# Kernel optimization log

Hardware: AMD Instinct MI355X
Metric: run time of the kernel (lower is better)

Reference implementation:

```python
import jax, jax.numpy as jnp
import numpy as np

SHAPE = (64, 64, 64)
N0 = 4000
K = 5  # subm conv kernel size -> 125 taps


def _neighbors(coors, shp):
    # coors: [N,4] int (b,z,y,x), batch=1. Returns [N,125] int32 neighbor row ids, -1 if absent.
    offs = np.stack(np.meshgrid(np.arange(-2, 3), np.arange(-2, 3), np.arange(-2, 3), indexing='ij'), -1).reshape(-1, 3)
    shp = np.asarray(shp)
    grid = -np.ones(tuple(shp), np.int32)
    grid[coors[:, 1], coors[:, 2], coors[:, 3]] = np.arange(len(coors), dtype=np.int32)
    nb = coors[:, None, 1:4] + offs[None]  # [N,125,3]
    valid = ((nb >= 0) & (nb < shp)).all(-1)
    nbc = np.clip(nb, 0, shp - 1)
    nbr = grid[nbc[..., 0], nbc[..., 1], nbc[..., 2]]
    return np.where(valid, nbr, -1).astype(np.int32)


def _pool_map(coors, shp):
    # kernel 2 stride 2 sparse max pool: parent cell = spatial // 2
    out_shp = [s // 2 for s in shp]
    sp = coors[:, 1:4] // 2
    lin = (sp[:, 0] * out_shp[1] + sp[:, 1]) * out_shp[2] + sp[:, 2]
    uniq, inv = np.unique(lin, return_inverse=True)
    z = uniq // (out_shp[1] * out_shp[2])
    r = uniq % (out_shp[1] * out_shp[2])
    nc = np.stack([np.zeros_like(z), z, r // out_shp[2], r % out_shp[2]], 1).astype(np.int32)
    return inv.astype(np.int32), nc, out_shp


_PAIRS = [(3, 64), (64, 64), (64, 96), (96, 96), (96, 128), (128, 128), (128, 160), (160, 160), (160, 192), (192, 192), (192, 224), (224, 224), (224, 256), (256, 256)]
_WNAMES = ['w0a', 'w0b', 'w1a', 'w1b', 'w2a', 'w2b', 'w3a', 'w3b', 'w4a', 'w4b', 'w5a', 'w5b', 'w6a', 'w6b']


def setup_inputs() -> dict:
    rng = np.random.RandomState(0)
    lin = rng.choice(SHAPE[0] * SHAPE[1] * SHAPE[2], N0, replace=False)
    z = lin // (SHAPE[1] * SHAPE[2])
    r = lin % (SHAPE[1] * SHAPE[2])
    coors = np.stack([np.zeros_like(z), z, r // SHAPE[2], r % SHAPE[2]], 1).astype(np.int32)
    inp = {}
    c, shp = coors, list(SHAPE)
    for l in range(7):
        inp['nbr%d' % l] = jnp.asarray(_neighbors(c, shp))
        if l < 6:
            pm, c, shp = _pool_map(c, shp)
            inp['pool%d' % l] = jnp.asarray(pm)
    key = jax.random.key(0)
    for name, (ci, co) in zip(_WNAMES, _PAIRS):
        key, k = jax.random.split(key)
        inp[name] = jax.random.normal(k, (K ** 3, ci, co), jnp.float32) * (K ** 3 * ci) ** -0.5
    key, kf = jax.random.split(key)
    inp['features'] = jax.random.normal(kf, (N0, 3), jnp.float32)
    inp['coors'] = jnp.asarray(coors)
    inp['batch_size'] = 1
    return inp


def _subm(feats, nbr, w):
    # gather-GEMM-scatter form of SubMConv3d (bias=False): out active set == in active set
    valid = nbr >= 0  # [N,125]
    g = jnp.take(feats, jnp.maximum(nbr, 0), axis=0)  # [N,125,Cin]
    g = jnp.where(valid[:, :, None], g, jnp.zeros((), feats.dtype))
    return jnp.einsum('nkc,kco->no', g, w)  # [N,Cout]


def reference(features, coors, batch_size, nbr0, nbr1, nbr2, nbr3, nbr4, nbr5, nbr6, pool0, pool1, pool2, pool3, pool4, pool5, w0a, w0b, w1a, w1b, w2a, w2b, w3a, w3b, w4a, w4b, w5a, w5b, w6a, w6b):
    nbrs = (nbr0, nbr1, nbr2, nbr3, nbr4, nbr5, nbr6)
    pools = (pool0, pool1, pool2, pool3, pool4, pool5)
    ws = ((w0a, w0b), (w1a, w1b), (w2a, w2b), (w3a, w3b), (w4a, w4b), (w5a, w5b), (w6a, w6b))
    x = features
    for l in range(7):
        x = _subm(x, nbrs[l], ws[l][0])
        x = _subm(x, nbrs[l], ws[l][1])
        if l < 6:
            # sparse max pool over active voxels of each 2x2x2 cell
            x = jax.ops.segment_max(x, pools[l], num_segments=nbrs[l + 1].shape[0])
    return x
```

## Files before the change

kernel.cpp:

```cpp
#include <hip/hip_runtime.h>
#include <stddef.h>
#include <stdint.h>

#define KTAPS 125

typedef _Float16 f16x8 __attribute__((ext_vector_type(8)));
typedef float    f32x4 __attribute__((ext_vector_type(4)));

template<int NT, bool F32IN>
__global__ __launch_bounds__(256) void subm_mfma(
    const void* __restrict__ fin, const int* __restrict__ nbr,
    const _Float16* __restrict__ wt, float* __restrict__ fout,
    int N, int CinP, int TS, int CS, float inscale, float outscale)
{
    constexpr int BN = NT * 32;
    __shared__ int       nbs[16][64];
    __shared__ unsigned  msk[16][2];
    __shared__ unsigned char vtl[2][16];
    __shared__ int       vcs[2];

    const int tid  = threadIdx.x;
    const int lane = tid & 63;
    const int wid  = tid >> 6;
    const int wy   = wid & 1;
    const int wx   = wid >> 1;
    const int r15  = lane & 15;
    const int g4   = lane >> 4;
    const int row0 = blockIdx.x * 64;
    const int k0   = (blockIdx.y * KTAPS) / TS;
    const int k1   = ((blockIdx.y + 1) * KTAPS) / TS;
    const int KR   = k1 - k0;
    const int CC   = CinP >> 5;
    const int cc0  = (blockIdx.z * CC) / CS;
    const int cc1  = ((blockIdx.z + 1) * CC) / CS;

    #pragma unroll
    for (int p = 0; p < 4; ++p) {
        int e = tid + p * 256;
        if (e < KR * 64) {
            int j = e >> 6, r = e & 63;
            int gr = row0 + r;
            nbs[j][r] = (gr < N) ? nbr[(size_t)gr * KTAPS + k0 + j] : -1;
        }
    }
    __syncthreads();
    for (int j = wid; j < KR; j += 4) {
        unsigned long long m = __ballot(nbs[j][lane] >= 0);
        if (lane == 0) { msk[j][0] = (unsigned)m; msk[j][1] = (unsigned)(m >> 32); }
    }
    __syncthreads();
    if (wid < 2) {
        int c = 0;
        for (int j = 0; j < KR; ++j)
            if (msk[j][wid]) { if (lane == 0) vtl[wid][c] = (unsigned char)j; ++c; }
        if (lane == 0) vcs[wid] = c;
    }
    __syncthreads();
    const int VCw = vcs[wy];
    if (VCw == 0) return;

    unsigned um = 0;
    for (int t = 0; t < VCw; ++t) um |= msk[vtl[wy][t]][wy];

    f32x4 acc[2][NT];
    #pragma unroll
    for (int mt = 0; mt < 2; ++mt)
        #pragma unroll
        for (int nf = 0; nf < NT; ++nf)
            acc[mt][nf] = (f32x4){0.f, 0.f, 0.f, 0.f};

    const size_t wchunk = (size_t)32 * BN;
    const int    boffh  = (g4 * BN + wx * (NT * 16) + r15) * 8;

    auto LOADA = [&](f16x8 (&a)[2], int j, int c) {
        #pragma unroll
        for (int mt = 0; mt < 2; ++mt) {
            int src = nbs[j][wy * 32 + mt * 16 + r15];
            if (src < 0) src = N;
            size_t base = (size_t)src * CinP + c * 32 + g4 * 8;
            if (F32IN) {
                const float* p = (const float*)fin + base;
                float4 v0 = *(const float4*)p;
                float4 v1 = *(const float4*)(p + 4);
                f16x8 h;
                h[0] = (_Float16)(v0.x * inscale); h[1] = (_Float16)(v0.y * inscale);
                h[2] = (_Float16)(v0.z * inscale); h[3] = (_Float16)(v0.w * inscale);
                h[4] = (_Float16)(v1.x * inscale); h[5] = (_Float16)(v1.y * inscale);
                h[6] = (_Float16)(v1.z * inscale); h[7] = (_Float16)(v1.w * inscale);
                a[mt] = h;
            } else {
                a[mt] = *(const f16x8*)((const _Float16*)fin + base);
            }
        }
    };
    auto LOADB = [&](f16x8 (&b)[NT], int j, int c) {
        const _Float16* base = wt + ((size_t)(k0 + j) * CC + c) * wchunk;
        #pragma unroll
        for (int nf = 0; nf < NT; ++nf)
            b[nf] = *(const f16x8*)&base[boffh + nf * 128];
    };
    auto MFMA = [&](f16x8 (&a)[2], f16x8 (&b)[NT]) {
        #pragma unroll
        for (int mt = 0; mt < 2; ++mt)
            #pragma unroll
            for (int nf = 0; nf < NT; ++nf)
                acc[mt][nf] = __builtin_amdgcn_mfma_f32_16x16x32_f16(a[mt], b[nf], acc[mt][nf], 0, 0, 0);
    };

    f16x8 a0[2], b0[NT], a1[2], b1[NT];
    int i = 0, c = cc0;
    { int j = vtl[wy][0]; LOADA(a0, j, c); LOADB(b0, j, c); }
    while (true) {
        int ni = i, nc = c + 1; if (nc == cc1) { ni = i + 1; nc = cc0; }
        bool m1 = ni < VCw;
        if (m1) { int j = vtl[wy][ni]; LOADA(a1, j, nc); LOADB(b1, j, nc); }
        MFMA(a0, b0);
        if (!m1) break;
        i = ni; c = nc;
        ni = i; nc = c + 1; if (nc == cc1) { ni = i + 1; nc = cc0; }
        bool m2 = ni < VCw;
        if (m2) { int j = vtl[wy][ni]; LOADA(a0, j, nc); LOADB(b0, j, nc); }
        MFMA(a1, b1);
        if (!m2) break;
        i = ni; c = nc;
    }

    #pragma unroll
    for (int mt = 0; mt < 2; ++mt) {
        #pragma unroll
        for (int q = 0; q < 4; ++q) {
            int lr = mt * 16 + g4 * 4 + q;
            int gr = row0 + wy * 32 + lr;
            if (((um >> lr) & 1u) && gr < N) {
                #pragma unroll
                for (int nf = 0; nf < NT; ++nf) {
                    int col = wx * (NT * 16) + nf * 16 + r15;
                    atomicAdd(&fout[(size_t)gr * BN + col], acc[mt][nf][q] * outscale);
                }
            }
        }
    }
}

__global__ __launch_bounds__(256) void tap_flags(
    const int* n0, const int* n1, const int* n2, const int* n3,
    const int* n4, const int* n5, const int* n6,
    int N0, int N1, int N2, int N3, int N4, int N5, int N6,
    unsigned* __restrict__ flags)
{
    int l = blockIdx.y, k = blockIdx.x;
    const int* nb; int N;
    switch (l) {
        case 0: nb = n0; N = N0; break;  case 1: nb = n1; N = N1; break;
        case 2: nb = n2; N = N2; break;  case 3: nb = n3; N = N3; break;
        case 4: nb = n4; N = N4; break;  case 5: nb = n5; N = N5; break;
        default: nb = n6; N = N6; break;
    }
    bool any = false;
    for (int r = threadIdx.x; r < N; r += 256) any |= (nb[(size_t)r * KTAPS + k] >= 0);
    bool a = __syncthreads_or(any);
    if (threadIdx.x == 0) flags[l * KTAPS + k] = a ? 1u : 0u;
}

__global__ __launch_bounds__(256) void cvt_weights(
    const float* __restrict__ wa, const float* __restrict__ wb,
    _Float16* __restrict__ ta, _Float16* __restrict__ tb,
    const unsigned* __restrict__ flags,
    int CinA, int CCa, int CoutA, int splitA,
    int CinB, int CCb, int CoutB)
{
    int k = blockIdx.x;
    if (!flags[k]) return;
    int by = blockIdx.y;
    const float* w; _Float16* t; int Cin, CC, Cout, cc, c0;
    if (by < splitA) { w = wa; t = ta; Cin = CinA; CC = CCa; Cout = CoutA;
                       cc = by / (CoutA / 32); c0 = (by % (CoutA / 32)) * 32; }
    else { by -= splitA; w = wb; t = tb; Cin = CinB; CC = CCb; Cout = CoutB;
           cc = by / (CoutB / 32); c0 = (by % (CoutB / 32)) * 32; }

    __shared__ float T[32][33];
    int tid = threadIdx.x;
    #pragma unroll
    for (int p = 0; p < 4; ++p) {
        int e = tid + p * 256;
        int r = e >> 5, cl = e & 31;
        int ci = cc * 32 + r;
        T[r][cl] = (ci < Cin) ? w[((size_t)k * Cin + ci) * Cout + c0 + cl] : 0.f;
    }
    __syncthreads();
    if (tid < 128) {
        int g = tid >> 5, co = tid & 31;
        f16x8 h;
        #pragma unroll
        for (int j = 0; j < 8; ++j) h[j] = (_Float16)T[g * 8 + j][co];
        *(f16x8*)&t[((size_t)k * CC + cc) * (32 * (size_t)Cout) + ((size_t)g * Cout + c0 + co) * 8] = h;
    }
}

__global__ __launch_bounds__(256) void init_all(
    const float* __restrict__ feat, _Float16* __restrict__ H,
    float* __restrict__ Fa, float* __restrict__ Fb,
    unsigned* __restrict__ ENC, float* __restrict__ dout,
    int N0, int nFa, int nFb, int nE, int nOut)
{
    int i = blockIdx.x * 256 + threadIdx.x;
    if (i < nFa) Fa[i] = 0.f;
    if (i < nFb) Fb[i] = 0.f;
    if (i < nE)  ENC[i] = 0u;
    if (i < nOut) dout[i] = 0.f;
    int nH = (N0 + 1) * 32;
    if (i < nH) {
        int r = i >> 5, cl = i & 31;
        H[i] = (r < N0 && cl < 3) ? (_Float16)feat[r * 3 + cl] : (_Float16)0.f;
    }
}

__device__ __forceinline__ unsigned enc_f32(float f) {
    unsigned u = __float_as_uint(f);
    return (u & 0x80000000u) ? ~u : (u | 0x80000000u);
}

__global__ __launch_bounds__(256) void pool_max(
    float* __restrict__ Fb, const int* __restrict__ pm,
    unsigned* __restrict__ ENC, float* __restrict__ Fa,
    int Nin, int C, int nzero)
{
    int i = blockIdx.x * 256 + threadIdx.x;
    if (i < Nin * C) {
        int r = i / C, cl = i - r * C;
        atomicMax(&ENC[(size_t)pm[r] * C + cl], enc_f32(Fb[i]));
        Fb[i] = 0.f;
    }
    if (i < nzero) Fa[i] = 0.f;
}

__global__ __launch_bounds__(256) void pool_dec(
    unsigned* __restrict__ ENC, _Float16* __restrict__ H, int Nout, int C, float scale)
{
    int i = blockIdx.x * 256 + threadIdx.x;
    if (i < Nout * C) {
        unsigned u = ENC[i];
        float f = __uint_as_float((u & 0x80000000u) ? (u ^ 0x80000000u) : ~u);
        H[i] = (_Float16)(f * scale);
        ENC[i] = 0u;
    } else if (i < (Nout + 1) * C) {
        H[i] = (_Float16)0.f;
    }
}

template<bool F32>
static void conv_dispatch(int NT, dim3 g, hipStream_t s, const void* fin, const int* nbr,
                          const _Float16* wt, float* fout, int N, int CinP, int TS, int CS,
                          float insc, float outsc)
{
    switch (NT) {
        case 2: subm_mfma<2,F32><<<g,256,0,s>>>(fin,nbr,wt,fout,N,CinP,TS,CS,insc,outsc); break;
        case 3: subm_mfma<3,F32><<<g,256,0,s>>>(fin,nbr,wt,fout,N,CinP,TS,CS,insc,outsc); break;
        case 4: subm_mfma<4,F32><<<g,256,0,s>>>(fin,nbr,wt,fout,N,CinP,TS,CS,insc,outsc); break;
        case 5: subm_mfma<5,F32><<<g,256,0,s>>>(fin,nbr,wt,fout,N,CinP,TS,CS,insc,outsc); break;
        case 6: subm_mfma<6,F32><<<g,256,0,s>>>(fin,nbr,wt,fout,N,CinP,TS,CS,insc,outsc); break;
        case 7: subm_mfma<7,F32><<<g,256,0,s>>>(fin,nbr,wt,fout,N,CinP,TS,CS,insc,outsc); break;
        case 8: subm_mfma<8,F32><<<g,256,0,s>>>(fin,nbr,wt,fout,N,CinP,TS,CS,insc,outsc); break;
    }
}

static void launch_conv(bool f32in, const void* fin, const int* nbr, const _Float16* wt,
                        float* fout, int N, int CinP, int Cout, float insc, float outsc,
                        hipStream_t s)
{
    int rt = (N + 63) / 64;
    int TS = (1536 + rt - 1) / rt;
    if (TS > KTAPS) TS = KTAPS;
    int CC = CinP / 32;
    int CS = 1;
    long blocks = (long)rt * TS;
    if (blocks < 1024) { CS = (int)((1536 + blocks - 1) / blocks); if (CS > CC) CS = CC; }
    dim3 g(rt, TS, CS);
    if (f32in) conv_dispatch<true >(Cout/32, g, s, fin, nbr, wt, fout, N, CinP, TS, CS, insc, outsc);
    else       conv_dispatch<false>(Cout/32, g, s, fin, nbr, wt, fout, N, CinP, TS, CS, insc, outsc);
}

extern "C" void kernel_launch(void* const* d_in, const int* in_sizes, int n_in,
                              void* d_out, int out_size, void* d_ws, size_t ws_size,
                              hipStream_t stream)
{
    const int* nbr[7]; const int* pm[6]; int Ns[7];
    {
        int idx = 0;
        for (int l = 0; l < 7; ++l) {
            nbr[l] = (const int*)d_in[idx];
            Ns[l]  = in_sizes[idx] / KTAPS;
            ++idx;
            if (l < 6) { pm[l] = (const int*)d_in[idx]; ++idx; }
        }
    }
    const float* w[14];
    for (int i = 0; i < 14; ++i) w[i] = (const float*)d_in[13 + i];
    const float* feat = (const float*)d_in[27];

    static const int CI[14]  = {3,64, 64,96, 96,128, 128,160, 160,192, 192,224, 224,256};
    static const int CO[14]  = {64,64, 96,96, 128,128, 160,160, 192,192, 224,224, 256,256};
    static const int KSH[14] = {0,3, 2,2, 1,1, 0,0, 0,1, 0,2, 2,3};
    const float finalScale = 1.0f / 131072.0f;
    int CinP[14];
    for (int i = 0; i < 14; ++i) CinP[i] = (CI[i] < 32) ? 32 : CI[i];

    size_t maxFa = 0, maxFb = 0, maxE = 0, maxHa = 0, maxWA = 0, maxWB = 0;
    for (int l = 0; l < 7; ++l) {
        size_t fa = (size_t)(Ns[l] + 1) * CO[2*l];   if (fa > maxFa) maxFa = fa;
        size_t fb = (size_t)(Ns[l] + 1) * CO[2*l+1]; if (fb > maxFb) maxFb = fb;
        if (l < 6) { size_t e = (size_t)Ns[l+1] * CO[2*l+1]; if (e > maxE) maxE = e; }
        size_t ha = (size_t)(Ns[l] + 1) * CinP[2*l]; if (ha > maxHa) maxHa = ha;
        size_t wa = (size_t)KTAPS * CinP[2*l] * CO[2*l];     if (wa > maxWA) maxWA = wa;
        size_t wb = (size_t)KTAPS * CinP[2*l+1] * CO[2*l+1]; if (wb > maxWB) maxWB = wb;
    }
    size_t off = 0;
    auto carve = [&](size_t bytes) -> void* {
        void* p = (char*)d_ws + off;
        off = (off + bytes + 255) & ~(size_t)255;
        return p;
    };
    float*     Fa   = (float*)carve(maxFa * 4);
    float*     Fb   = (float*)carve(maxFb * 4);
    unsigned*  ENC  = (unsigned*)carve(maxE * 4);
    _Float16*  Ha   = (_Float16*)carve(maxHa * 2);
    _Float16*  wtA  = (_Float16*)carve(maxWA * 2);
    _Float16*  wtB  = (_Float16*)carve(maxWB * 2);
    unsigned*  flags= (unsigned*)carve(7 * KTAPS * 4);

    {
        int nMax = (int)maxFa;
        if ((int)maxFb > nMax) nMax = (int)maxFb;
        if ((int)maxE  > nMax) nMax = (int)maxE;
        int nH = (Ns[0] + 1) * 32;
        if (nH > nMax) nMax = nH;
        if (out_size > nMax) nMax = out_size;
        init_all<<<(nMax + 255) / 256, 256, 0, stream>>>(
            feat, Ha, Fa, Fb, ENC, (float*)d_out,
            Ns[0], (int)maxFa, (int)maxFb, (int)maxE, out_size);
    }
    tap_flags<<<dim3(KTAPS, 7), 256, 0, stream>>>(
        nbr[0], nbr[1], nbr[2], nbr[3], nbr[4], nbr[5], nbr[6],
        Ns[0], Ns[1], Ns[2], Ns[3], Ns[4], Ns[5], Ns[6], flags);

    for (int l = 0; l < 7; ++l) {
        int ia = 2 * l, ib = 2 * l + 1;
        int N = Ns[l];
        int splitA = (CinP[ia] / 32) * (CO[ia] / 32);
        int splitB = (CinP[ib] / 32) * (CO[ib] / 32);
        cvt_weights<<<dim3(KTAPS, splitA + splitB), 256, 0, stream>>>(
            w[ia], w[ib], wtA, wtB, flags + l * KTAPS,
            CI[ia], CinP[ia] / 32, CO[ia], splitA,
            CI[ib], CinP[ib] / 32, CO[ib]);

        launch_conv(false, Ha, nbr[l], wtA, Fa, N, CinP[ia], CO[ia], 1.f, 1.f, stream);

        float* outb = (l == 6) ? (float*)d_out : Fb;
        launch_conv(true, Fa, nbr[l], wtB, outb, N, CinP[ib], CO[ib],
                    (float)(1 << KSH[ib]), (l == 6) ? finalScale : 1.f, stream);

        if (l < 6) {
            int C = CO[ib], Nout = Ns[l + 1];
            int nzero = (Nout + 1) * CO[2 * l + 2];
            int tot = N * C; if (nzero > tot) tot = nzero;
            pool_max<<<(tot + 255) / 256, 256, 0, stream>>>(Fb, pm[l], ENC, Fa, N, C, nzero);
            int tot2 = (Nout + 1) * C;
            pool_dec<<<(tot2 + 255) / 256, 256, 0, stream>>>(ENC, Ha, Nout, C,
                                                             (float)(1 << KSH[2 * l + 2]));
        }
    }
}
```

Before: 427.2 us.

## Replace atomic split-K accumulation with per-split partial buffers and reduction kernels

The sparse conv kernel no longer uses atomicAdd into fp32 output. Each tap-split block now writes plain stores into its own partial-sum slice. New reduce kernels sum the slices, and they also fuse the fp16 conversion for the next conv and the encoded max-pool atomics, which removes the separate pool_max pass and the zeroing of accumulators. The channel-split grid dimension is dropped, and MFMAs and A-loads for all-empty 16-row halves are skipped. The cost is writing and re-reading TS×N×C fp32 partials, plus a different split-count heuristic.

```diff
diff --git a/kernel.cpp b/kernel.cpp
--- a/kernel.cpp
+++ b/kernel.cpp
@@ -3,15 +3,17 @@
 #include <stdint.h>
 
 #define KTAPS 125
+#define TARGET_BLOCKS 512
 
 typedef _Float16 f16x8 __attribute__((ext_vector_type(8)));
+typedef _Float16 f16x4 __attribute__((ext_vector_type(4)));
 typedef float    f32x4 __attribute__((ext_vector_type(4)));
 
-template<int NT, bool F32IN>
+template<int NT>
 __global__ __launch_bounds__(256) void subm_mfma(
-    const void* __restrict__ fin, const int* __restrict__ nbr,
-    const _Float16* __restrict__ wt, float* __restrict__ fout,
-    int N, int CinP, int TS, int CS, float inscale, float outscale)
+    const _Float16* __restrict__ finh, const int* __restrict__ nbr,
+    const _Float16* __restrict__ wt, float* __restrict__ Pout,
+    int N, int CinP, int TS)
 {
     constexpr int BN = NT * 32;
     __shared__ int       nbs[16][64];
@@ -31,8 +33,6 @@
     const int k1   = ((blockIdx.y + 1) * KTAPS) / TS;
     const int KR   = k1 - k0;
     const int CC   = CinP >> 5;
-    const int cc0  = (blockIdx.z * CC) / CS;
-    const int cc1  = ((blockIdx.z + 1) * CC) / CS;
 
     #pragma unroll
     for (int p = 0; p < 4; ++p) {
@@ -57,10 +57,6 @@
     }
     __syncthreads();
     const int VCw = vcs[wy];
-    if (VCw == 0) return;
-
-    unsigned um = 0;
-    for (int t = 0; t < VCw; ++t) um |= msk[vtl[wy][t]][wy];
 
     f32x4 acc[2][NT];
     #pragma unroll
@@ -69,76 +65,138 @@
         for (int nf = 0; nf < NT; ++nf)
             acc[mt][nf] = (f32x4){0.f, 0.f, 0.f, 0.f};
 
-    const size_t wchunk = (size_t)32 * BN;
-    const int    boffh  = (g4 * BN + wx * (NT * 16) + r15) * 8;
-
-    auto LOADA = [&](f16x8 (&a)[2], int j, int c) {
-        #pragma unroll
-        for (int mt = 0; mt < 2; ++mt) {
-            int src = nbs[j][wy * 32 + mt * 16 + r15];
-            if (src < 0) src = N;
-            size_t base = (size_t)src * CinP + c * 32 + g4 * 8;
-            if (F32IN) {
-                const float* p = (const float*)fin + base;
-                float4 v0 = *(const float4*)p;
-                float4 v1 = *(const float4*)(p + 4);
-                f16x8 h;
-                h[0] = (_Float16)(v0.x * inscale); h[1] = (_Float16)(v0.y * inscale);
-                h[2] = (_Float16)(v0.z * inscale); h[3] = (_Float16)(v0.w * inscale);
-                h[4] = (_Float16)(v1.x * inscale); h[5] = (_Float16)(v1.y * inscale);
-                h[6] = (_Float16)(v1.z * inscale); h[7] = (_Float16)(v1.w * inscale);
-                a[mt] = h;
-            } else {
-                a[mt] = *(const f16x8*)((const _Float16*)fin + base);
+    if (VCw > 0) {
+        const size_t wchunk = (size_t)32 * BN;
+        const int    boffh  = (g4 * BN + wx * (NT * 16) + r15) * 8;
+
+        auto LOADA = [&](f16x8 (&a)[2], int j, int c) {
+            unsigned mm = __builtin_amdgcn_readfirstlane(msk[j][wy]);
+            if (mm & 0xFFFFu) {
+                int src = nbs[j][wy * 32 + r15];
+                if (src < 0) src = N;
+                a[0] = *(const f16x8*)(finh + (size_t)src * CinP + c * 32 + g4 * 8);
             }
-        }
-    };
-    auto LOADB = [&](f16x8 (&b)[NT], int j, int c) {
-        const _Float16* base = wt + ((size_t)(k0 + j) * CC + c) * wchunk;
-        #pragma unroll
-        for (int nf = 0; nf < NT; ++nf)
-            b[nf] = *(const f16x8*)&base[boffh + nf * 128];
-    };
-    auto MFMA = [&](f16x8 (&a)[2], f16x8 (&b)[NT]) {
-        #pragma unroll
-        for (int mt = 0; mt < 2; ++mt)
+            if (mm >> 16) {
+                int src = nbs[j][wy * 32 + 16 + r15];
+                if (src < 0) src = N;
+                a[1] = *(const f16x8*)(finh + (size_t)src * CinP + c * 32 + g4 * 8);
+            }
+        };
+        auto LOADB = [&](f16x8 (&b)[NT], int j, int c) {
+            const _Float16* base = wt + ((size_t)(k0 + j) * CC + c) * wchunk;
             #pragma unroll
             for (int nf = 0; nf < NT; ++nf)
-                acc[mt][nf] = __builtin_amdgcn_mfma_f32_16x16x32_f16(a[mt], b[nf], acc[mt][nf], 0, 0, 0);
-    };
-
-    f16x8 a0[2], b0[NT], a1[2], b1[NT];
-    int i = 0, c = cc0;
-    { int j = vtl[wy][0]; LOADA(a0, j, c); LOADB(b0, j, c); }
-    while (true) {
-        int ni = i, nc = c + 1; if (nc == cc1) { ni = i + 1; nc = cc0; }
-        bool m1 = ni < VCw;
-        if (m1) { int j = vtl[wy][ni]; LOADA(a1, j, nc); LOADB(b1, j, nc); }
-        MFMA(a0, b0);
-        if (!m1) break;
-        i = ni; c = nc;
-        ni = i; nc = c + 1; if (nc == cc1) { ni = i + 1; nc = cc0; }
-        bool m2 = ni < VCw;
-        if (m2) { int j = vtl[wy][ni]; LOADA(a0, j, nc); LOADB(b0, j, nc); }
-        MFMA(a1, b1);
-        if (!m2) break;
-        i = ni; c = nc;
-    }
-
+                b[nf] = *(const f16x8*)&base[boffh + nf * 128];
+        };
+        auto DOMFMA = [&](f16x8 (&a)[2], f16x8 (&b)[NT], int j) {
+            unsigned mm = __builtin_amdgcn_readfirstlane(msk[j][wy]);
+            if (mm & 0xFFFFu)
+                #pragma unroll
+                for (int nf = 0; nf < NT; ++nf)
+                    acc[0][nf] = __builtin_amdgcn_mfma_f32_16x16x32_f16(a[0], b[nf], acc[0][nf], 0, 0, 0);
+            if (mm >> 16)
+                #pragma unroll
+                for (int nf = 0; nf < NT; ++nf)
+                    acc[1][nf] = __builtin_amdgcn_mfma_f32_16x16x32_f16(a[1], b[nf], acc[1][nf], 0, 0, 0);
+        };
+
+        f16x8 a0[2], b0[NT], a1[2], b1[NT];
+        int i = 0, c = 0;
+        int jA = vtl[wy][0], jB = 0;
+        LOADA(a0, jA, 0); LOADB(b0, jA, 0);
+        while (true) {
+            int ni = i, nc = c + 1; if (nc == CC) { ni = i + 1; nc = 0; }
+            bool m1 = ni < VCw;
+            if (m1) { jB = vtl[wy][ni]; LOADA(a1, jB, nc); LOADB(b1, jB, nc); }
+            DOMFMA(a0, b0, jA);
+            if (!m1) break;
+            i = ni; c = nc;
+            ni = i; nc = c + 1; if (nc == CC) { ni = i + 1; nc = 0; }
+            bool m2 = ni < VCw;
+            if (m2) { jA = vtl[wy][ni]; LOADA(a0, jA, nc); LOADB(b0, jA, nc); }
+            DOMFMA(a1, b1, jB);
+            if (!m2) break;
+            i = ni; c = nc;
+        }
+    }
+
+    float* base = Pout + (size_t)blockIdx.y * ((size_t)N * BN);
     #pragma unroll
     for (int mt = 0; mt < 2; ++mt) {
         #pragma unroll
         for (int q = 0; q < 4; ++q) {
-            int lr = mt * 16 + g4 * 4 + q;
-            int gr = row0 + wy * 32 + lr;
-            if (((um >> lr) & 1u) && gr < N) {
+            int r = row0 + wy * 32 + mt * 16 + g4 * 4 + q;
+            if (r < N) {
                 #pragma unroll
-                for (int nf = 0; nf < NT; ++nf) {
-                    int col = wx * (NT * 16) + nf * 16 + r15;
-                    atomicAdd(&fout[(size_t)gr * BN + col], acc[mt][nf][q] * outscale);
-                }
+                for (int nf = 0; nf < NT; ++nf)
+                    base[(size_t)r * BN + wx * (NT * 16) + nf * 16 + r15] = acc[mt][nf][q];
             }
         }
+    }
+}
+
+__global__ __launch_bounds__(256) void reduce_a(
+    const float* __restrict__ P, _Float16* __restrict__ H,
+    int N, int BN, int S, float scale)
+{
+    int idx = blockIdx.x * 256 + threadIdx.x;
+    size_t i4 = (size_t)idx * 4;
+    if (i4 >= (size_t)(N + 1) * BN) return;
+    f16x4 h;
+    if (i4 >= (size_t)N * BN) {
+        h[0] = h[1] = h[2] = h[3] = (_Float16)0.f;
+    } else {
+        f32x4 s = *(const f32x4*)&P[i4];
+        size_t stride = (size_t)N * BN;
+        for (int si = 1; si < S; ++si)
+            s += *(const f32x4*)&P[si * stride + i4];
+        h[0] = (_Float16)(s[0] * scale); h[1] = (_Float16)(s[1] * scale);
+        h[2] = (_Float16)(s[2] * scale); h[3] = (_Float16)(s[3] * scale);
+    }
+    *(f16x4*)&H[i4] = h;
+}
+
+__device__ __forceinline__ unsigned enc_f32(float f) {
+    unsigned u = __float_as_uint(f);
+    return (u & 0x80000000u) ? ~u : (u | 0x80000000u);
+}
+
+__global__ __launch_bounds__(256) void reduce_b(
+    const float* __restrict__ P, const int* __restrict__ pm,
+    unsigned* __restrict__ ENC, float* __restrict__ dout,
+    int N, int BN, int S, float fscale, int isLast)
+{
+    int idx = blockIdx.x * 256 + threadIdx.x;
+    size_t i4 = (size_t)idx * 4;
+    if (i4 >= (size_t)N * BN) return;
+    f32x4 s = *(const f32x4*)&P[i4];
+    size_t stride = (size_t)N * BN;
+    for (int si = 1; si < S; ++si)
+        s += *(const f32x4*)&P[si * stride + i4];
+    if (isLast) {
+        dout[i4 + 0] = s[0] * fscale; dout[i4 + 1] = s[1] * fscale;
+        dout[i4 + 2] = s[2] * fscale; dout[i4 + 3] = s[3] * fscale;
+    } else {
+        int row = (int)(i4 / BN), c = (int)(i4 % BN);
+        unsigned* e = &ENC[(size_t)pm[row] * BN + c];
+        atomicMax(e + 0, enc_f32(s[0]));
+        atomicMax(e + 1, enc_f32(s[1]));
+        atomicMax(e + 2, enc_f32(s[2]));
+        atomicMax(e + 3, enc_f32(s[3]));
+    }
+}
+
+__global__ __launch_bounds__(256) void pool_dec(
+    unsigned* __restrict__ ENC, _Float16* __restrict__ H, int Nout, int C, float scale)
+{
+    int i = blockIdx.x * 256 + threadIdx.x;
+    if (i < Nout * C) {
+        unsigned u = ENC[i];
+        float f = __uint_as_float((u & 0x80000000u) ? (u ^ 0x80000000u) : ~u);
+        H[i] = (_Float16)(f * scale);
+        ENC[i] = 0u;
+    } else if (i < (Nout + 1) * C) {
+        H[i] = (_Float16)0.f;
     }
 }
 
@@ -199,15 +257,10 @@
 
 __global__ __launch_bounds__(256) void init_all(
     const float* __restrict__ feat, _Float16* __restrict__ H,
-    float* __restrict__ Fa, float* __restrict__ Fb,
-    unsigned* __restrict__ ENC, float* __restrict__ dout,
-    int N0, int nFa, int nFb, int nE, int nOut)
+    unsigned* __restrict__ ENC, int N0, int nE)
 {
     int i = blockIdx.x * 256 + threadIdx.x;
-    if (i < nFa) Fa[i] = 0.f;
-    if (i < nFb) Fb[i] = 0.f;
-    if (i < nE)  ENC[i] = 0u;
-    if (i < nOut) dout[i] = 0.f;
+    if (i < nE) ENC[i] = 0u;
     int nH = (N0 + 1) * 32;
     if (i < nH) {
         int r = i >> 5, cl = i & 31;
@@ -215,69 +268,26 @@
     }
 }
 
-__device__ __forceinline__ unsigned enc_f32(float f) {
-    unsigned u = __float_as_uint(f);
-    return (u & 0x80000000u) ? ~u : (u | 0x80000000u);
-}
-
-__global__ __launch_bounds__(256) void pool_max(
-    float* __restrict__ Fb, const int* __restrict__ pm,
-    unsigned* __restrict__ ENC, float* __restrict__ Fa,
-    int Nin, int C, int nzero)
-{
-    int i = blockIdx.x * 256 + threadIdx.x;
-    if (i < Nin * C) {
-        int r = i / C, cl = i - r * C;
-        atomicMax(&ENC[(size_t)pm[r] * C + cl], enc_f32(Fb[i]));
-        Fb[i] = 0.f;
-    }
-    if (i < nzero) Fa[i] = 0.f;
-}
-
-__global__ __launch_bounds__(256) void pool_dec(
-    unsigned* __restrict__ ENC, _Float16* __restrict__ H, int Nout, int C, float scale)
-{
-    int i = blockIdx.x * 256 + threadIdx.x;
-    if (i < Nout * C) {
-        unsigned u = ENC[i];
-        float f = __uint_as_float((u & 0x80000000u) ? (u ^ 0x80000000u) : ~u);
-        H[i] = (_Float16)(f * scale);
-        ENC[i] = 0u;
-    } else if (i < (Nout + 1) * C) {
-        H[i] = (_Float16)0.f;
-    }
-}
-
-template<bool F32>
-static void conv_dispatch(int NT, dim3 g, hipStream_t s, const void* fin, const int* nbr,
-                          const _Float16* wt, float* fout, int N, int CinP, int TS, int CS,
-                          float insc, float outsc)
+static inline int pick_ts(int rt)
+{
+    int ts = (TARGET_BLOCKS + rt - 1) / rt;
+    if (ts < 8) ts = 8;
+    if (ts > KTAPS) ts = KTAPS;
+    return ts;
+}
+
+static void conv_dispatch(int NT, dim3 g, hipStream_t s, const _Float16* fin, const int* nbr,
+                          const _Float16* wt, float* P, int N, int CinP, int TS)
 {
     switch (NT) {
-        case 2: subm_mfma<2,F32><<<g,256,0,s>>>(fin,nbr,wt,fout,N,CinP,TS,CS,insc,outsc); break;
-        case 3: subm_mfma<3,F32><<<g,256,0,s>>>(fin,nbr,wt,fout,N,CinP,TS,CS,insc,outsc); break;
-        case 4: subm_mfma<4,F32><<<g,256,0,s>>>(fin,nbr,wt,fout,N,CinP,TS,CS,insc,outsc); break;
-        case 5: subm_mfma<5,F32><<<g,256,0,s>>>(fin,nbr,wt,fout,N,CinP,TS,CS,insc,outsc); break;
-        case 6: subm_mfma<6,F32><<<g,256,0,s>>>(fin,nbr,wt,fout,N,CinP,TS,CS,insc,outsc); break;
-        case 7: subm_mfma<7,F32><<<g,256,0,s>>>(fin,nbr,wt,fout,N,CinP,TS,CS,insc,outsc); break;
-        case 8: subm_mfma<8,F32><<<g,256,0,s>>>(fin,nbr,wt,fout,N,CinP,TS,CS,insc,outsc); break;
-    }
-}
-
-static void launch_conv(bool f32in, const void* fin, const int* nbr, const _Float16* wt,
-                        float* fout, int N, int CinP, int Cout, float insc, float outsc,
-                        hipStream_t s)
-{
-    int rt = (N + 63) / 64;
-    int TS = (1536 + rt - 1) / rt;
-    if (TS > KTAPS) TS = KTAPS;
-    int CC = CinP / 32;
-    int CS = 1;
-    long blocks = (long)rt * TS;
-    if (blocks < 1024) { CS = (int)((1536 + blocks - 1) / blocks); if (CS > CC) CS = CC; }
-    dim3 g(rt, TS, CS);
-    if (f32in) conv_dispatch<true >(Cout/32, g, s, fin, nbr, wt, fout, N, CinP, TS, CS, insc, outsc);
-    else       conv_dispatch<false>(Cout/32, g, s, fin, nbr, wt, fout, N, CinP, TS, CS, insc, outsc);
+        case 2: subm_mfma<2><<<g,256,0,s>>>(fin,nbr,wt,P,N,CinP,TS); break;
+        case 3: subm_mfma<3><<<g,256,0,s>>>(fin,nbr,wt,P,N,CinP,TS); break;
+        case 4: subm_mfma<4><<<g,256,0,s>>>(fin,nbr,wt,P,N,CinP,TS); break;
+        case 5: subm_mfma<5><<<g,256,0,s>>>(fin,nbr,wt,P,N,CinP,TS); break;
+        case 6: subm_mfma<6><<<g,256,0,s>>>(fin,nbr,wt,P,N,CinP,TS); break;
+        case 7: subm_mfma<7><<<g,256,0,s>>>(fin,nbr,wt,P,N,CinP,TS); break;
+        case 8: subm_mfma<8><<<g,256,0,s>>>(fin,nbr,wt,P,N,CinP,TS); break;
+    }
 }
 
 extern "C" void kernel_launch(void* const* d_in, const int* in_sizes, int n_in,
@@ -305,12 +315,17 @@
     int CinP[14];
     for (int i = 0; i < 14; ++i) CinP[i] = (CI[i] < 32) ? 32 : CI[i];
 
-    size_t maxFa = 0, maxFb = 0, maxE = 0, maxHa = 0, maxWA = 0, maxWB = 0;
+    int TSv[14];
+    size_t maxP = 0, maxHa = 0, maxHb = 0, maxE = 0, maxWA = 0, maxWB = 0;
     for (int l = 0; l < 7; ++l) {
-        size_t fa = (size_t)(Ns[l] + 1) * CO[2*l];   if (fa > maxFa) maxFa = fa;
-        size_t fb = (size_t)(Ns[l] + 1) * CO[2*l+1]; if (fb > maxFb) maxFb = fb;
+        int rt = (Ns[l] + 63) / 64;
+        int ts = pick_ts(rt);
+        TSv[2*l] = ts; TSv[2*l+1] = ts;
+        size_t pa = (size_t)ts * Ns[l] * CO[2*l];   if (pa > maxP) maxP = pa;
+        size_t pb = (size_t)ts * Ns[l] * CO[2*l+1]; if (pb > maxP) maxP = pb;
+        size_t ha = (size_t)(Ns[l] + 1) * CinP[2*l];   if (ha > maxHa) maxHa = ha;
+        size_t hb = (size_t)(Ns[l] + 1) * CinP[2*l+1]; if (hb > maxHb) maxHb = hb;
         if (l < 6) { size_t e = (size_t)Ns[l+1] * CO[2*l+1]; if (e > maxE) maxE = e; }
-        size_t ha = (size_t)(Ns[l] + 1) * CinP[2*l]; if (ha > maxHa) maxHa = ha;
         size_t wa = (size_t)KTAPS * CinP[2*l] * CO[2*l];     if (wa > maxWA) maxWA = wa;
         size_t wb = (size_t)KTAPS * CinP[2*l+1] * CO[2*l+1]; if (wb > maxWB) maxWB = wb;
     }
@@ -320,24 +335,19 @@
         off = (off + bytes + 255) & ~(size_t)255;
         return p;
     };
-    float*     Fa   = (float*)carve(maxFa * 4);
-    float*     Fb   = (float*)carve(maxFb * 4);
+    float*     P    = (float*)carve(maxP * 4);
+    _Float16*  Ha   = (_Float16*)carve(maxHa * 2);
+    _Float16*  Hb   = (_Float16*)carve(maxHb * 2);
     unsigned*  ENC  = (unsigned*)carve(maxE * 4);
-    _Float16*  Ha   = (_Float16*)carve(maxHa * 2);
     _Float16*  wtA  = (_Float16*)carve(maxWA * 2);
     _Float16*  wtB  = (_Float16*)carve(maxWB * 2);
     unsigned*  flags= (unsigned*)carve(7 * KTAPS * 4);
 
     {
-        int nMax = (int)maxFa;
-        if ((int)maxFb > nMax) nMax = (int)maxFb;
-        if ((int)maxE  > nMax) nMax = (int)maxE;
+        int nMax = (int)maxE;
         int nH = (Ns[0] + 1) * 32;
         if (nH > nMax) nMax = nH;
-        if (out_size > nMax) nMax = out_size;
-        init_all<<<(nMax + 255) / 256, 256, 0, stream>>>(
-            feat, Ha, Fa, Fb, ENC, (float*)d_out,
-            Ns[0], (int)maxFa, (int)maxFb, (int)maxE, out_size);
+        init_all<<<(nMax + 255) / 256, 256, 0, stream>>>(feat, Ha, ENC, Ns[0], (int)maxE);
     }
     tap_flags<<<dim3(KTAPS, 7), 256, 0, stream>>>(
         nbr[0], nbr[1], nbr[2], nbr[3], nbr[4], nbr[5], nbr[6],
@@ -346,6 +356,7 @@
     for (int l = 0; l < 7; ++l) {
         int ia = 2 * l, ib = 2 * l + 1;
         int N = Ns[l];
+        int rt = (N + 63) / 64;
         int splitA = (CinP[ia] / 32) * (CO[ia] / 32);
         int splitB = (CinP[ib] / 32) * (CO[ib] / 32);
         cvt_weights<<<dim3(KTAPS, splitA + splitB), 256, 0, stream>>>(
@@ -353,17 +364,23 @@
             CI[ia], CinP[ia] / 32, CO[ia], splitA,
             CI[ib], CinP[ib] / 32, CO[ib]);
 
-        launch_conv(false, Ha, nbr[l], wtA, Fa, N, CinP[ia], CO[ia], 1.f, 1.f, stream);
-
-        float* outb = (l == 6) ? (float*)d_out : Fb;
-        launch_conv(true, Fa, nbr[l], wtB, outb, N, CinP[ib], CO[ib],
-                    (float)(1 << KSH[ib]), (l == 6) ? finalScale : 1.f, stream);
-
+        {
+            int TS = TSv[ia], BN = CO[ia];
+            conv_dispatch(BN / 32, dim3(rt, TS), stream, Ha, nbr[l], wtA, P, N, CinP[ia], TS);
+            int tot = ((N + 1) * BN + 3) / 4;
+            reduce_a<<<(tot + 255) / 256, 256, 0, stream>>>(P, Hb, N, BN, TS,
+                                                            (float)(1 << KSH[ib]));
+        }
+        {
+            int TS = TSv[ib], BN = CO[ib];
+            conv_dispatch(BN / 32, dim3(rt, TS), stream, Hb, nbr[l], wtB, P, N, CinP[ib], TS);
+            int tot = (N * BN + 3) / 4;
+            reduce_b<<<(tot + 255) / 256, 256, 0, stream>>>(
+                P, (l < 6) ? pm[l] : nullptr, ENC, (float*)d_out,
+                N, BN, TS, finalScale, (l == 6) ? 1 : 0);
+        }
         if (l < 6) {
             int C = CO[ib], Nout = Ns[l + 1];
-            int nzero = (Nout + 1) * CO[2 * l + 2];
-            int tot = N * C; if (nzero > tot) tot = nzero;
-            pool_max<<<(tot + 255) / 256, 256, 0, stream>>>(Fb, pm[l], ENC, Fa, N, C, nzero);
             int tot2 = (Nout + 1) * C;
             pool_dec<<<(tot2 + 255) / 256, 256, 0, stream>>>(ENC, Ha, Nout, C,
                                                              (float)(1 << KSH[2 * l + 2]));
```

Result: slower. 559.5 us (+31.0%).
